# Kernel tuning notes

Measured on AMD Instinct MI355X. Metric: run time of the kernel, lower is better.

## Reference

```python
import jax, jax.numpy as jnp
import numpy as np

N_NODES = 100000
N_EDGES = 1600000
IN_CH = 128


def _glorot(key, shape):
    fan_in, fan_out = shape[0], shape[1]
    lim = float(np.sqrt(6.0 / (fan_in + fan_out)))
    return jax.random.uniform(key, shape, jnp.float32, -lim, lim)


def setup_inputs() -> dict:
    key = jax.random.key(0)
    ks = jax.random.split(key, 12)
    x = jax.random.normal(ks[0], (N_NODES, IN_CH), jnp.float32)
    edge_index = jax.random.randint(ks[1], (2, N_EDGES), 0, N_NODES, jnp.int64)
    # conv1: lin2 (in->64), lin1 (2*64 -> 64)
    W2_1 = _glorot(ks[2], (IN_CH, 64)); b2_1 = jnp.zeros((64,), jnp.float32)
    W1_1 = _glorot(ks[3], (128, 64));   b1_1 = jnp.zeros((64,), jnp.float32)
    # conv2: lin2 (64->32), lin1 (2*32 -> 32)
    W2_2 = _glorot(ks[4], (64, 32));    b2_2 = jnp.zeros((32,), jnp.float32)
    W1_2 = _glorot(ks[5], (64, 32));    b1_2 = jnp.zeros((32,), jnp.float32)
    # final lin (32 -> 1)
    Wl = _glorot(ks[6], (32, 1));       bl = jnp.zeros((1,), jnp.float32)
    return {"x": x, "edge_index": edge_index,
            "W2_1": W2_1, "b2_1": b2_1, "W1_1": W1_1, "b1_1": b1_1,
            "W2_2": W2_2, "b2_2": b2_2, "W1_2": W1_2, "b1_2": b1_2,
            "Wl": Wl, "bl": bl}


def _feat_graph_conv(x, src, dst, n, W2, b2, W1, b1):
    # h = lin2(x)
    h = x @ W2 + b2                          # [N, hidden]
    # message: h_j gathered at edge source (edge_weight is None -> identity)
    msg = h[src]                              # [E+N, hidden]
    # scatter-mean aggregation onto destination nodes
    agg = jax.ops.segment_sum(msg, dst, num_segments=n)          # [N, hidden]
    cnt = jax.ops.segment_sum(jnp.ones_like(dst, jnp.float32), dst, num_segments=n)
    agg = agg / jnp.maximum(cnt, 1.0)[:, None]
    # update: lin1(concat(h, agg))
    return jnp.concatenate((h, agg), axis=1) @ W1 + b1


def reference(x, edge_index, W2_1, b2_1, W1_1, b1_1,
              W2_2, b2_2, W1_2, b1_2, Wl, bl):
    n = x.shape[0]
    loops = jnp.arange(n, dtype=edge_index.dtype)
    src = jnp.concatenate((edge_index[0], loops))  # add self loops
    dst = jnp.concatenate((edge_index[1], loops))
    h1 = jax.nn.relu(_feat_graph_conv(x, src, dst, n, W2_1, b2_1, W1_1, b1_1))
    h2 = jax.nn.relu(_feat_graph_conv(h1, src, dst, n, W2_2, b2_2, W1_2, b1_2))
    return h2 @ Wl + bl                       # [N, 1]
```

## Files before the change

### kernel.cpp

```cpp
#include <hip/hip_runtime.h>

#define N_NODES 100000
#define N_EDGES 1600000
constexpr int BLK = 256;
constexpr int NBKT = (N_NODES + 127) / 128;
constexpr int BCAP = 4096;
constexpr int PACK_SHIFT = 17;
constexpr int EPT = 16;
constexpr int EPBLK = BLK * EPT;
constexpr int NSCAT = (N_EDGES + EPBLK - 1) / EPBLK;

__device__ __forceinline__ unsigned short f2bf(float f) {
    unsigned int u = __float_as_uint(f);
    u = (u + 0x7FFFu + ((u >> 16) & 1u)) >> 16;
    return (unsigned short)u;
}
__device__ __forceinline__ float bf2f(unsigned short s) {
    return __uint_as_float(((unsigned int)s) << 16);
}

__global__ void detect_idx64(const unsigned int* __restrict__ e, int* __restrict__ flag) {
    if (blockIdx.x == 0 && threadIdx.x == 0) {
        int is64 = 1;
        for (int i = 0; i < 64; ++i) if (e[2 * i + 1] != 0u) { is64 = 0; break; }
        *flag = is64;
    }
}

__device__ __forceinline__ int load_dst(const int* e, int f, int i) {
    return f ? e[2 * (N_EDGES + i)] : e[N_EDGES + i];
}
__device__ __forceinline__ int load_src(const int* e, int f, int i) {
    return f ? e[2 * i] : e[i];
}

__global__ void bucket_scatter(const int* __restrict__ eraw, const int* __restrict__ flag,
                               int* __restrict__ cursor, int* __restrict__ ebkt) {
    __shared__ int h[NBKT];
    const int f = *flag;
    const int e0 = blockIdx.x * EPBLK;
    for (int i = threadIdx.x; i < NBKT; i += BLK) h[i] = 0;
    __syncthreads();
    int bs[EPT], ps[EPT];
#pragma unroll
    for (int k = 0; k < EPT; ++k) {
        const int i = e0 + k * BLK + threadIdx.x;
        if (i < N_EDGES) {
            const int d = load_dst(eraw, f, i);
            const int s = load_src(eraw, f, i);
            bs[k] = d >> 7;
            ps[k] = s | ((d & 127) << PACK_SHIFT);
            atomicAdd(&h[bs[k]], 1);
        } else {
            bs[k] = -1;
            ps[k] = 0;
        }
    }
    __syncthreads();
    for (int b = threadIdx.x; b < NBKT; b += BLK) {
        const int c = h[b];
        if (c) h[b] = atomicAdd(&cursor[b], c);
    }
    __syncthreads();
#pragma unroll
    for (int k = 0; k < EPT; ++k) {
        if (bs[k] >= 0) {
            const int off = atomicAdd(&h[bs[k]], 1);
            ebkt[bs[k] * BCAP + off] = ps[k];
        }
    }
}

__global__ void csrify(const int* __restrict__ cnt_b, const int* __restrict__ ebkt,
                       int* __restrict__ adj, int* __restrict__ rowptr,
                       int* __restrict__ deg) {
    __shared__ int hist[128];
    __shared__ int excl[128];
    __shared__ int lcur[128];
    const int b = blockIdx.x;
    const int s0 = b * BCAP;
    const int s1 = s0 + cnt_b[b];
    for (int i = threadIdx.x; i < 128; i += BLK) hist[i] = 0;
    __syncthreads();
    for (int i = s0 + threadIdx.x; i < s1; i += BLK)
        atomicAdd(&hist[ebkt[i] >> PACK_SHIFT], 1);
    __syncthreads();
    if (threadIdx.x < 128) excl[threadIdx.x] = hist[threadIdx.x];
    __syncthreads();
    for (int off = 1; off < 128; off <<= 1) {
        int t = 0;
        if (threadIdx.x < 128 && threadIdx.x >= off) t = excl[threadIdx.x - off];
        __syncthreads();
        if (threadIdx.x < 128) excl[threadIdx.x] += t;
        __syncthreads();
    }
    if (threadIdx.x < 128) {
        const int e = excl[threadIdx.x] - hist[threadIdx.x];
        lcur[threadIdx.x] = s0 + e;
        const int node = b * 128 + threadIdx.x;
        if (node < N_NODES) {
            rowptr[node] = s0 + e;
            deg[node] = hist[threadIdx.x];
        }
    }
    __syncthreads();
    for (int i = s0 + threadIdx.x; i < s1; i += BLK) {
        const int p = ebkt[i];
        const int pos = atomicAdd(&lcur[p >> PACK_SHIFT], 1);
        adj[pos] = p & ((1 << PACK_SHIFT) - 1);
    }
}

__device__ __forceinline__ void fma_step(float4& acc, float xs, float4 w) {
    acc.x = fmaf(xs, w.x, acc.x);
    acc.y = fmaf(xs, w.y, acc.y);
    acc.z = fmaf(xs, w.z, acc.z);
    acc.w = fmaf(xs, w.w, acc.w);
}

__device__ __forceinline__ void add4(float4& a, float4 v) {
    a.x += v.x; a.y += v.y; a.z += v.z; a.w += v.w;
}

__device__ __forceinline__ void addbf4(float4& a, ushort4 t) {
    a.x += bf2f(t.x); a.y += bf2f(t.y); a.z += bf2f(t.z); a.w += bf2f(t.w);
}

template<int K, int C>
__global__ void gemm_bias(const float* __restrict__ X, const float* __restrict__ W,
                          const float* __restrict__ bias, float* __restrict__ Y,
                          unsigned short* __restrict__ Yb, int n) {
    constexpr int CQ = C / 4;
    constexpr int NPB = BLK / CQ;
    constexpr int KQ = K / 4;
    __shared__ float4 Ws[K * CQ];
    __shared__ float4 xL[NPB * KQ];
    for (int i = threadIdx.x; i < K * CQ; i += BLK)
        Ws[i] = reinterpret_cast<const float4*>(W)[i];
    const int cq = threadIdx.x % CQ;
    const int ns = threadIdx.x / CQ;
    const float4 bv = reinterpret_cast<const float4*>(bias)[cq];
    const float4* X4 = reinterpret_cast<const float4*>(X);
    const int tile = blockIdx.x;
    for (int i = threadIdx.x; i < NPB * KQ; i += BLK) {
        const int r = i / KQ;
        const int k4 = i % KQ;
        xL[r * KQ + ((k4 + r) % KQ)] = X4[(size_t)(tile * NPB + r) * KQ + k4];
    }
    __syncthreads();
    const float4* xr = &xL[ns * KQ];
    float4 acc = bv;
#pragma unroll 4
    for (int k4 = 0; k4 < KQ; ++k4) {
        float4 xv = xr[(k4 + ns) % KQ];
        fma_step(acc, xv.x, Ws[(4 * k4 + 0) * CQ + cq]);
        fma_step(acc, xv.y, Ws[(4 * k4 + 1) * CQ + cq]);
        fma_step(acc, xv.z, Ws[(4 * k4 + 2) * CQ + cq]);
        fma_step(acc, xv.w, Ws[(4 * k4 + 3) * CQ + cq]);
    }
    const size_t oi = (size_t)(tile * NPB + ns) * CQ + cq;
    reinterpret_cast<float4*>(Y)[oi] = acc;
    ushort4 bfv;
    bfv.x = f2bf(acc.x); bfv.y = f2bf(acc.y);
    bfv.z = f2bf(acc.z); bfv.w = f2bf(acc.w);
    reinterpret_cast<ushort4*>(Yb)[oi] = bfv;
}

template<int KH, int C, int TPB>
__global__ void update_gather(const float* __restrict__ P,
                              const unsigned short* __restrict__ Pb,
                              const int* __restrict__ rowptr, const int* __restrict__ cnt,
                              const int* __restrict__ adj,
                              const float* __restrict__ W, const float* __restrict__ bias,
                              float* __restrict__ Y, int n) {
    constexpr int CQ = C / 4;
    constexpr int NPB = TPB / CQ;
    constexpr int K = 2 * KH;
    __shared__ float4 Ws[K * CQ];
    __shared__ float4 Ag[NPB][CQ + 1];
    for (int i = threadIdx.x; i < K * CQ; i += TPB)
        Ws[i] = reinterpret_cast<const float4*>(W)[i];
    __syncthreads();
    const int cq = threadIdx.x % CQ;
    const int ns = threadIdx.x / CQ;
    const float4 bv = reinterpret_cast<const float4*>(bias)[cq];
    const float4* P4 = reinterpret_cast<const float4*>(P);
    const ushort4* Pb4 = reinterpret_cast<const ushort4*>(Pb);
    const int node = blockIdx.x * NPB + ns;
    const int start = rowptr[node];
    const int deg = cnt[node];
    const float inv = 1.0f / (float)(deg + 1);
    const float4* pr = &P4[(size_t)node * CQ];

    float4 agg = {0.f, 0.f, 0.f, 0.f};
    int j = 0;
    for (; j + 7 < deg; j += 8) {
        const int s0 = adj[start + j];
        const int s1 = adj[start + j + 1];
        const int s2 = adj[start + j + 2];
        const int s3 = adj[start + j + 3];
        const int s4 = adj[start + j + 4];
        const int s5 = adj[start + j + 5];
        const int s6 = adj[start + j + 6];
        const int s7 = adj[start + j + 7];
        const ushort4 t0 = Pb4[(size_t)s0 * CQ + cq];
        const ushort4 t1 = Pb4[(size_t)s1 * CQ + cq];
        const ushort4 t2 = Pb4[(size_t)s2 * CQ + cq];
        const ushort4 t3 = Pb4[(size_t)s3 * CQ + cq];
        const ushort4 t4 = Pb4[(size_t)s4 * CQ + cq];
        const ushort4 t5 = Pb4[(size_t)s5 * CQ + cq];
        const ushort4 t6 = Pb4[(size_t)s6 * CQ + cq];
        const ushort4 t7 = Pb4[(size_t)s7 * CQ + cq];
        addbf4(agg, t0); addbf4(agg, t1); addbf4(agg, t2); addbf4(agg, t3);
        addbf4(agg, t4); addbf4(agg, t5); addbf4(agg, t6); addbf4(agg, t7);
    }
    if (j + 3 < deg) {
        const int s0 = adj[start + j];
        const int s1 = adj[start + j + 1];
        const int s2 = adj[start + j + 2];
        const int s3 = adj[start + j + 3];
        const ushort4 t0 = Pb4[(size_t)s0 * CQ + cq];
        const ushort4 t1 = Pb4[(size_t)s1 * CQ + cq];
        const ushort4 t2 = Pb4[(size_t)s2 * CQ + cq];
        const ushort4 t3 = Pb4[(size_t)s3 * CQ + cq];
        addbf4(agg, t0); addbf4(agg, t1); addbf4(agg, t2); addbf4(agg, t3);
        j += 4;
    }
    for (; j < deg; ++j)
        addbf4(agg, Pb4[(size_t)adj[start + j] * CQ + cq]);

    float4 acc = bv;
#pragma unroll 4
    for (int k4 = 0; k4 < KH / 4; ++k4) {
        float4 pv = pr[k4];
        fma_step(acc, pv.x, Ws[(4 * k4 + 0) * CQ + cq]);
        fma_step(acc, pv.y, Ws[(4 * k4 + 1) * CQ + cq]);
        fma_step(acc, pv.z, Ws[(4 * k4 + 2) * CQ + cq]);
        fma_step(acc, pv.w, Ws[(4 * k4 + 3) * CQ + cq]);
    }
    {
        float4 pv = pr[cq];
        add4(agg, pv);
        agg.x *= inv; agg.y *= inv; agg.z *= inv; agg.w *= inv;
    }
    Ag[ns][cq] = agg;
    __syncthreads();
#pragma unroll 4
    for (int k4 = 0; k4 < KH / 4; ++k4) {
        float4 av = Ag[ns][k4];
        fma_step(acc, av.x, Ws[(KH + 4 * k4 + 0) * CQ + cq]);
        fma_step(acc, av.y, Ws[(KH + 4 * k4 + 1) * CQ + cq]);
        fma_step(acc, av.z, Ws[(KH + 4 * k4 + 2) * CQ + cq]);
        fma_step(acc, av.w, Ws[(KH + 4 * k4 + 3) * CQ + cq]);
    }
    acc.x = fmaxf(acc.x, 0.0f);
    acc.y = fmaxf(acc.y, 0.0f);
    acc.z = fmaxf(acc.z, 0.0f);
    acc.w = fmaxf(acc.w, 0.0f);
    reinterpret_cast<float4*>(Y)[(size_t)node * CQ + cq] = acc;
}

__global__ void update2_final(const float* __restrict__ P,
                              const unsigned short* __restrict__ Pb,
                              const int* __restrict__ rowptr, const int* __restrict__ cnt,
                              const int* __restrict__ adj,
                              const float* __restrict__ W, const float* __restrict__ bias,
                              const float* __restrict__ Wl, const float* __restrict__ bl,
                              float* __restrict__ out, int n) {
    constexpr int CQ = 8;
    constexpr int NPB = BLK / CQ;
    __shared__ float4 Ws[64 * CQ];
    __shared__ float4 Ag[NPB][CQ + 1];
    for (int i = threadIdx.x; i < 64 * CQ; i += BLK)
        Ws[i] = reinterpret_cast<const float4*>(W)[i];
    __syncthreads();
    const int cq = threadIdx.x % CQ;
    const int ns = threadIdx.x / CQ;
    const float4 bv = reinterpret_cast<const float4*>(bias)[cq];
    const float4 wlv = reinterpret_cast<const float4*>(Wl)[cq];
    const float blv = bl[0];
    const float4* P4 = reinterpret_cast<const float4*>(P);
    const ushort4* Pb4 = reinterpret_cast<const ushort4*>(Pb);
    const int node = blockIdx.x * NPB + ns;
    const int start = rowptr[node];
    const int deg = cnt[node];
    const float inv = 1.0f / (float)(deg + 1);
    const float4* pr = &P4[(size_t)node * CQ];

    float4 agg = {0.f, 0.f, 0.f, 0.f};
    int j = 0;
    for (; j + 7 < deg; j += 8) {
        const int s0 = adj[start + j];
        const int s1 = adj[start + j + 1];
        const int s2 = adj[start + j + 2];
        const int s3 = adj[start + j + 3];
        const int s4 = adj[start + j + 4];
        const int s5 = adj[start + j + 5];
        const int s6 = adj[start + j + 6];
        const int s7 = adj[start + j + 7];
        const ushort4 t0 = Pb4[(size_t)s0 * CQ + cq];
        const ushort4 t1 = Pb4[(size_t)s1 * CQ + cq];
        const ushort4 t2 = Pb4[(size_t)s2 * CQ + cq];
        const ushort4 t3 = Pb4[(size_t)s3 * CQ + cq];
        const ushort4 t4 = Pb4[(size_t)s4 * CQ + cq];
        const ushort4 t5 = Pb4[(size_t)s5 * CQ + cq];
        const ushort4 t6 = Pb4[(size_t)s6 * CQ + cq];
        const ushort4 t7 = Pb4[(size_t)s7 * CQ + cq];
        addbf4(agg, t0); addbf4(agg, t1); addbf4(agg, t2); addbf4(agg, t3);
        addbf4(agg, t4); addbf4(agg, t5); addbf4(agg, t6); addbf4(agg, t7);
    }
    if (j + 3 < deg) {
        const int s0 = adj[start + j];
        const int s1 = adj[start + j + 1];
        const int s2 = adj[start + j + 2];
        const int s3 = adj[start + j + 3];
        const ushort4 t0 = Pb4[(size_t)s0 * CQ + cq];
        const ushort4 t1 = Pb4[(size_t)s1 * CQ + cq];
        const ushort4 t2 = Pb4[(size_t)s2 * CQ + cq];
        const ushort4 t3 = Pb4[(size_t)s3 * CQ + cq];
        addbf4(agg, t0); addbf4(agg, t1); addbf4(agg, t2); addbf4(agg, t3);
        j += 4;
    }
    for (; j < deg; ++j)
        addbf4(agg, Pb4[(size_t)adj[start + j] * CQ + cq]);

    float4 acc = bv;
#pragma unroll
    for (int k4 = 0; k4 < 8; ++k4) {
        float4 pv = pr[k4];
        fma_step(acc, pv.x, Ws[(4 * k4 + 0) * CQ + cq]);
        fma_step(acc, pv.y, Ws[(4 * k4 + 1) * CQ + cq]);
        fma_step(acc, pv.z, Ws[(4 * k4 + 2) * CQ + cq]);
        fma_step(acc, pv.w, Ws[(4 * k4 + 3) * CQ + cq]);
    }
    {
        float4 pv = pr[cq];
        add4(agg, pv);
        agg.x *= inv; agg.y *= inv; agg.z *= inv; agg.w *= inv;
    }
    Ag[ns][cq] = agg;
    __syncthreads();
#pragma unroll
    for (int k4 = 0; k4 < 8; ++k4) {
        float4 av = Ag[ns][k4];
        fma_step(acc, av.x, Ws[(32 + 4 * k4 + 0) * CQ + cq]);
        fma_step(acc, av.y, Ws[(32 + 4 * k4 + 1) * CQ + cq]);
        fma_step(acc, av.z, Ws[(32 + 4 * k4 + 2) * CQ + cq]);
        fma_step(acc, av.w, Ws[(32 + 4 * k4 + 3) * CQ + cq]);
    }
    float v = fmaxf(acc.x, 0.0f) * wlv.x + fmaxf(acc.y, 0.0f) * wlv.y
            + fmaxf(acc.z, 0.0f) * wlv.z + fmaxf(acc.w, 0.0f) * wlv.w;
    v += __shfl_xor(v, 4, 8);
    v += __shfl_xor(v, 2, 8);
    v += __shfl_xor(v, 1, 8);
    if (cq == 0) out[node] = v + blv;
}

extern "C" void kernel_launch(void* const* d_in, const int* in_sizes, int n_in,
                              void* d_out, int out_size, void* d_ws, size_t ws_size,
                              hipStream_t stream) {
    const float* x    = (const float*)d_in[0];
    const int*   eraw = (const int*)d_in[1];
    const float* W2_1 = (const float*)d_in[2];
    const float* b2_1 = (const float*)d_in[3];
    const float* W1_1 = (const float*)d_in[4];
    const float* b1_1 = (const float*)d_in[5];
    const float* W2_2 = (const float*)d_in[6];
    const float* b2_2 = (const float*)d_in[7];
    const float* W1_2 = (const float*)d_in[8];
    const float* b1_2 = (const float*)d_in[9];
    const float* Wl   = (const float*)d_in[10];
    const float* bl   = (const float*)d_in[11];
    float* out = (float*)d_out;

    char* ws = (char*)d_ws;
    int* flag   = (int*)ws;
    size_t off = 256;
    int* cursor = (int*)(ws + off); off += sizeof(int) * (size_t)(NBKT + 2);
    off = (off + 255) & ~(size_t)255;
    int* ebkt   = (int*)(ws + off); off += sizeof(int) * (size_t)NBKT * BCAP;
    off = (off + 255) & ~(size_t)255;
    int* adj    = (int*)(ws + off); off += sizeof(int) * (size_t)NBKT * BCAP;
    int* rowptr = (int*)(ws + off); off += sizeof(int) * (size_t)N_NODES;
    int* deg    = (int*)(ws + off); off += sizeof(int) * (size_t)N_NODES;
    off = (off + 255) & ~(size_t)255;
    float* bufA = (float*)(ws + off); off += sizeof(float) * (size_t)N_NODES * 64;
    float* bufC = (float*)(ws + off); off += sizeof(float) * (size_t)N_NODES * 64;
    unsigned short* bufAb = (unsigned short*)(ws + off);
    off += sizeof(unsigned short) * (size_t)N_NODES * 64;

    hipMemsetAsync(cursor, 0, sizeof(int) * (size_t)(NBKT + 2), stream);

    detect_idx64<<<1, 64, 0, stream>>>((const unsigned int*)eraw, flag);
    bucket_scatter<<<NSCAT, BLK, 0, stream>>>(eraw, flag, cursor, ebkt);
    csrify<<<NBKT, BLK, 0, stream>>>(cursor, ebkt, adj, rowptr, deg);

    gemm_bias<128, 64><<<N_NODES / 16, BLK, 0, stream>>>(x, W2_1, b2_1, bufA, bufAb, N_NODES);
    update_gather<64, 64, 512><<<N_NODES / 32, 512, 0, stream>>>(bufA, bufAb, rowptr, deg, adj, W1_1, b1_1, bufC, N_NODES);

    gemm_bias<64, 32><<<N_NODES / 32, BLK, 0, stream>>>(bufC, W2_2, b2_2, bufA, bufAb, N_NODES);
    update2_final<<<N_NODES / 32, BLK, 0, stream>>>(bufA, bufAb, rowptr, deg, adj, W1_2, b1_2, Wl, bl, out, N_NODES);
}
```

Baseline: 191.7 us.

## Co-schedule first-layer GEMM with edge scatter and CSR build kernels

Splits the first-layer node GEMM into two halves and merges each half into the bucket-scatter and CSR-build launches, using blockIdx ranges to pick the role. This removes one kernel launch and lets the compute-bound GEMM blocks overlap the atomic-heavy, memory-bound graph preprocessing. Shared memory is unified to one buffer sized for the larger user, which may reduce occupancy for the scatter and CSR blocks.

```diff
diff --git a/kernel.cpp b/kernel.cpp
--- a/kernel.cpp
+++ b/kernel.cpp
@@ -9,6 +9,8 @@
 constexpr int EPT = 16;
 constexpr int EPBLK = BLK * EPT;
 constexpr int NSCAT = (N_EDGES + EPBLK - 1) / EPBLK;
+constexpr int GTILES = N_NODES / 16;
+constexpr int GHALF = GTILES / 2;
 
 __device__ __forceinline__ unsigned short f2bf(float f) {
     unsigned int u = __float_as_uint(f);
@@ -34,11 +36,25 @@
     return f ? e[2 * i] : e[i];
 }
 
-__global__ void bucket_scatter(const int* __restrict__ eraw, const int* __restrict__ flag,
-                               int* __restrict__ cursor, int* __restrict__ ebkt) {
-    __shared__ int h[NBKT];
-    const int f = *flag;
-    const int e0 = blockIdx.x * EPBLK;
+__device__ __forceinline__ void fma_step(float4& acc, float xs, float4 w) {
+    acc.x = fmaf(xs, w.x, acc.x);
+    acc.y = fmaf(xs, w.y, acc.y);
+    acc.z = fmaf(xs, w.z, acc.z);
+    acc.w = fmaf(xs, w.w, acc.w);
+}
+__device__ __forceinline__ void add4(float4& a, float4 v) {
+    a.x += v.x; a.y += v.y; a.z += v.z; a.w += v.w;
+}
+__device__ __forceinline__ void addbf4(float4& a, ushort4 t) {
+    a.x += bf2f(t.x); a.y += bf2f(t.y); a.z += bf2f(t.z); a.w += bf2f(t.w);
+}
+
+
+__device__ void scatter_body(const int* __restrict__ eraw, int f,
+                             int* __restrict__ cursor, int* __restrict__ ebkt,
+                             int bid, void* smem) {
+    int* h = (int*)smem;
+    const int e0 = bid * EPBLK;
     for (int i = threadIdx.x; i < NBKT; i += BLK) h[i] = 0;
     __syncthreads();
     int bs[EPT], ps[EPT];
@@ -71,13 +87,12 @@
     }
 }
 
-__global__ void csrify(const int* __restrict__ cnt_b, const int* __restrict__ ebkt,
-                       int* __restrict__ adj, int* __restrict__ rowptr,
-                       int* __restrict__ deg) {
-    __shared__ int hist[128];
-    __shared__ int excl[128];
-    __shared__ int lcur[128];
-    const int b = blockIdx.x;
+__device__ void csrify_body(const int* __restrict__ cnt_b, const int* __restrict__ ebkt,
+                            int* __restrict__ adj, int* __restrict__ rowptr,
+                            int* __restrict__ deg, int b, void* smem) {
+    int* hist = (int*)smem;
+    int* excl = hist + 128;
+    int* lcur = hist + 256;
     const int s0 = b * BCAP;
     const int s1 = s0 + cnt_b[b];
     for (int i = threadIdx.x; i < 128; i += BLK) hist[i] = 0;
@@ -111,19 +126,70 @@
     }
 }
 
-__device__ __forceinline__ void fma_step(float4& acc, float xs, float4 w) {
-    acc.x = fmaf(xs, w.x, acc.x);
-    acc.y = fmaf(xs, w.y, acc.y);
-    acc.z = fmaf(xs, w.z, acc.z);
-    acc.w = fmaf(xs, w.w, acc.w);
-}
-
-__device__ __forceinline__ void add4(float4& a, float4 v) {
-    a.x += v.x; a.y += v.y; a.z += v.z; a.w += v.w;
-}
-
-__device__ __forceinline__ void addbf4(float4& a, ushort4 t) {
-    a.x += bf2f(t.x); a.y += bf2f(t.y); a.z += bf2f(t.z); a.w += bf2f(t.w);
+template<int K, int C>
+__device__ void gemm_body(const float* __restrict__ X, const float* __restrict__ W,
+                          const float* __restrict__ bias, float* __restrict__ Y,
+                          unsigned short* __restrict__ Yb, int tile, void* smem) {
+    constexpr int CQ = C / 4;
+    constexpr int NPB = BLK / CQ;
+    constexpr int KQ = K / 4;
+    float4* Ws = (float4*)smem;
+    float4* xL = Ws + K * CQ;
+    for (int i = threadIdx.x; i < K * CQ; i += BLK)
+        Ws[i] = reinterpret_cast<const float4*>(W)[i];
+    const int cq = threadIdx.x % CQ;
+    const int ns = threadIdx.x / CQ;
+    const float4 bv = reinterpret_cast<const float4*>(bias)[cq];
+    const float4* X4 = reinterpret_cast<const float4*>(X);
+    for (int i = threadIdx.x; i < NPB * KQ; i += BLK) {
+        const int r = i / KQ;
+        const int k4 = i % KQ;
+        xL[r * KQ + ((k4 + r) % KQ)] = X4[(size_t)(tile * NPB + r) * KQ + k4];
+    }
+    __syncthreads();
+    const float4* xr = &xL[ns * KQ];
+    float4 acc = bv;
+#pragma unroll 4
+    for (int k4 = 0; k4 < KQ; ++k4) {
+        float4 xv = xr[(k4 + ns) % KQ];
+        fma_step(acc, xv.x, Ws[(4 * k4 + 0) * CQ + cq]);
+        fma_step(acc, xv.y, Ws[(4 * k4 + 1) * CQ + cq]);
+        fma_step(acc, xv.z, Ws[(4 * k4 + 2) * CQ + cq]);
+        fma_step(acc, xv.w, Ws[(4 * k4 + 3) * CQ + cq]);
+    }
+    const size_t oi = (size_t)(tile * NPB + ns) * CQ + cq;
+    reinterpret_cast<float4*>(Y)[oi] = acc;
+    ushort4 bfv;
+    bfv.x = f2bf(acc.x); bfv.y = f2bf(acc.y);
+    bfv.z = f2bf(acc.z); bfv.w = f2bf(acc.w);
+    reinterpret_cast<ushort4*>(Yb)[oi] = bfv;
+}
+
+__global__ void scatter_gemm(const int* __restrict__ eraw, const int* __restrict__ flag,
+                             int* __restrict__ cursor, int* __restrict__ ebkt,
+                             const float* __restrict__ X, const float* __restrict__ W,
+                             const float* __restrict__ bias, float* __restrict__ Y,
+                             unsigned short* __restrict__ Yb) {
+    __shared__ float4 smem[2560];
+    if (blockIdx.x < NSCAT) {
+        scatter_body(eraw, *flag, cursor, ebkt, blockIdx.x, smem);
+    } else {
+        gemm_body<128, 64>(X, W, bias, Y, Yb, blockIdx.x - NSCAT, smem);
+    }
+}
+
+__global__ void csrify_gemm(const int* __restrict__ cnt_b, const int* __restrict__ ebkt,
+                            int* __restrict__ adj, int* __restrict__ rowptr,
+                            int* __restrict__ deg,
+                            const float* __restrict__ X, const float* __restrict__ W,
+                            const float* __restrict__ bias, float* __restrict__ Y,
+                            unsigned short* __restrict__ Yb) {
+    __shared__ float4 smem[2560];
+    if (blockIdx.x < NBKT) {
+        csrify_body(cnt_b, ebkt, adj, rowptr, deg, blockIdx.x, smem);
+    } else {
+        gemm_body<128, 64>(X, W, bias, Y, Yb, GHALF + (int)blockIdx.x - NBKT, smem);
+    }
 }
 
 template<int K, int C>
@@ -392,10 +458,12 @@
     hipMemsetAsync(cursor, 0, sizeof(int) * (size_t)(NBKT + 2), stream);
 
     detect_idx64<<<1, 64, 0, stream>>>((const unsigned int*)eraw, flag);
-    bucket_scatter<<<NSCAT, BLK, 0, stream>>>(eraw, flag, cursor, ebkt);
-    csrify<<<NBKT, BLK, 0, stream>>>(cursor, ebkt, adj, rowptr, deg);
-
-    gemm_bias<128, 64><<<N_NODES / 16, BLK, 0, stream>>>(x, W2_1, b2_1, bufA, bufAb, N_NODES);
+
+    scatter_gemm<<<NSCAT + GHALF, BLK, 0, stream>>>(eraw, flag, cursor, ebkt,
+                                                    x, W2_1, b2_1, bufA, bufAb);
+    csrify_gemm<<<NBKT + GHALF, BLK, 0, stream>>>(cursor, ebkt, adj, rowptr, deg,
+                                                  x, W2_1, b2_1, bufA, bufAb);
+
     update_gather<64, 64, 512><<<N_NODES / 32, 512, 0, stream>>>(bufA, bufAb, rowptr, deg, adj, W1_1, b1_1, bufC, N_NODES);
 
     gemm_bias<64, 32><<<N_NODES / 32, BLK, 0, stream>>>(bufC, W2_2, b2_2, bufA, bufAb, N_NODES);
```

Result: faster. 187.0 us (-2.4%).
